# Kernel tuning notes

Hardware: AMD Instinct MI355X
Metric: run time of the kernel (lower is better)

The kernel has to match this reference:

```python
import jax, jax.numpy as jnp
import numpy as np

K = 12
ORDERS = [(1, 2, 3), (1, 3, 2), (3, 2, 1), (3, 1, 2), (2, 1, 3), (2, 3, 1)]


def ranking_3d(x):
    # x: (B, L1, W1, H1, D) -> (B, 12, L1*W1*H1, D)
    B, L1, W1, H1, D = x.shape
    seqs = []
    for dims in ORDERS:
        perm = (0,) + dims + (4,)
        seqs.append(jnp.transpose(x, perm).reshape(B, -1, D))
        xr = jnp.flip(x, axis=dims)
        seqs.append(jnp.transpose(xr, perm).reshape(B, -1, D))
    return jnp.stack(seqs, axis=1)


def restore_original(out_y, shape):
    # out_y: (B, 12, D, L). NOTE: faithfully replicates the original code, which
    # reshapes the (B, D, L) slice directly to (B, d1, d2, d3, D).
    B, L1, W1, H1, D = shape
    size = {1: L1, 2: W1, 3: H1}
    restored = []
    for i in range(12):
        dims = ORDERS[i // 2]
        seq = out_y[:, i]  # (B, D, L)
        dims_shape = tuple(size[d] for d in dims)
        reshaped = seq.reshape((B,) + dims_shape + (D,))
        perm = (0,) + dims + (4,)
        inv = tuple(np.argsort(perm))
        r = jnp.transpose(reshaped, inv)
        if i % 2 == 1:
            r = jnp.flip(r, axis=dims)
        restored.append(r)
    return restored


def selective_scan(u, delta, A, Bs, Cs):
    # u, delta: (B,K,D,L); A: (K,D,N); Bs, Cs: (B,K,N,L)
    us = jnp.moveaxis(u, -1, 0)       # (L,B,K,D)
    ds = jnp.moveaxis(delta, -1, 0)   # (L,B,K,D)
    Bts = jnp.moveaxis(Bs, -1, 0)     # (L,B,K,N)
    Cts = jnp.moveaxis(Cs, -1, 0)     # (L,B,K,N)
    h0 = jnp.zeros(u.shape[:-1] + (A.shape[-1],), u.dtype)  # (B,K,D,N)

    def step(h, inp):
        ut, dt, Bt, Ct = inp
        dA = jnp.exp(dt[..., None] * A)                       # (B,K,D,N)
        h = dA * h + (dt * ut)[..., None] * Bt[:, :, None, :]
        y = jnp.einsum('bkdn,bkn->bkd', h, Ct)
        return h, y

    _, ys = jax.lax.scan(step, h0, (us, ds, Bts, Cts))
    return jnp.moveaxis(ys, 0, -1)  # (B,K,D,L)


def setup_inputs() -> dict:
    key = jax.random.key(0)
    ks = jax.random.split(key, 8)
    B, H, W, Len, D = 1, 16, 16, 16, 128
    N, R = 16, 8
    x = jax.random.normal(ks[0], (B, H, W, Len, D), dtype=jnp.float32)
    x_proj_weight = jax.random.normal(ks[1], (K, R + 2 * N, D), dtype=jnp.float32) * 0.02
    std = R ** -0.5
    dt_projs_weight = jax.random.uniform(ks[2], (K, D, R), minval=-std, maxval=std, dtype=jnp.float32)
    dt = jnp.exp(jax.random.uniform(ks[3], (K, D)) * (np.log(0.1) - np.log(0.001)) + np.log(0.001))
    dt = jnp.clip(dt, 1e-4, None)
    dt_projs_bias = (dt + jnp.log(-jnp.expm1(-dt))).astype(jnp.float32)
    A_logs = jnp.broadcast_to(jnp.log(jnp.arange(1, N + 1, dtype=jnp.float32)), (K, D, N)).copy()
    Ds = jnp.ones((K, D), dtype=jnp.float32)
    merge_w = jax.random.normal(ks[4], (K,), dtype=jnp.float32) * (1.0 / K)
    merge_b = jax.random.normal(ks[5], (), dtype=jnp.float32) * 0.01
    return {'x': x, 'x_proj_weight': x_proj_weight, 'dt_projs_weight': dt_projs_weight,
            'dt_projs_bias': dt_projs_bias, 'A_logs': A_logs, 'Ds': Ds,
            'merge_w': merge_w, 'merge_b': merge_b}


def reference(x, x_proj_weight, dt_projs_weight, dt_projs_bias, A_logs, Ds, merge_w, merge_b):
    B, H, W, Len, D = x.shape
    L = H * W * Len
    R = dt_projs_weight.shape[-1]
    N = A_logs.shape[-1]
    xs = jnp.transpose(ranking_3d(x), (0, 1, 3, 2))  # (B,K,D,L)
    x_dbl = jnp.einsum('bkdl,kcd->bkcl', xs, x_proj_weight)  # (B,K,R+2N,L)
    dts, Bs, Cs = jnp.split(x_dbl, [R, R + N], axis=2)
    dts = jnp.einsum('bkrl,kdr->bkdl', dts, dt_projs_weight)
    delta = jax.nn.softplus(dts + dt_projs_bias[None, :, :, None])
    A = -jnp.exp(A_logs)  # (K,D,N)
    ys = selective_scan(xs, delta, A, Bs, Cs)
    out_y = ys + Ds[None, :, :, None] * xs  # (B,K,D,L)
    restored = restore_original(out_y, (B, H, W, Len, D))
    stacked = jnp.stack(restored, axis=1)  # (B,K,H,W,Len,D)
    # mergeconv: 1x1 Conv2d over K channels == weighted sum across directions
    y = jnp.einsum('bkhwld,k->bhwld', stacked, merge_w) + merge_b
    return y
```

## Files before the change

kernel.cpp:

```cpp
#include <hip/hip_runtime.h>

#define KK 12
#define LL 4096
#define DD 128
#define NN 16
#define RR 8
#define NC 128
#define LC 32

__device__ __forceinline__ int pos_of(int k, int l) {
    int o = k >> 1;
    int le = (k & 1) ? (4095 - l) : l;
    int t1 = le >> 8, t2 = (le >> 4) & 15, t3 = le & 15;
    switch (o) {
        case 0:  return (t1 << 8) | (t2 << 4) | t3;
        case 1:  return (t1 << 8) | (t3 << 4) | t2;
        case 2:  return (t3 << 8) | (t2 << 4) | t1;
        case 3:  return (t2 << 8) | (t3 << 4) | t1;
        case 4:  return (t2 << 8) | (t1 << 4) | t3;
        default: return (t3 << 8) | (t1 << 4) | t2;
    }
}

__device__ __forceinline__ float softplus_f(float z) {
    return fmaxf(z, 0.0f) + __logf(1.0f + __expf(-fabsf(z)));
}

__global__ __launch_bounds__(256) void proj_kernel(
    const float* __restrict__ x, const float* __restrict__ Wp,
    const float* __restrict__ Wdt, const float* __restrict__ bias,
    float* __restrict__ delta, float* __restrict__ Bc, float* __restrict__ Cc)
{
    int k = blockIdx.x >> 6;
    int l0 = (blockIdx.x & 63) * 64;
    int t = threadIdx.x;

    __shared__ float xs_s[64 * 132];

    {
        int lane32 = t & 31;
        int rowi = t >> 5;
        #pragma unroll
        for (int p = 0; p < 8; p++) {
            int l = p * 8 + rowi;
            int xbase = pos_of(k, l0 + l) * DD;
            float4 v = *(const float4*)(x + xbase + lane32 * 4);
            *(float4*)(&xs_s[l * 132 + lane32 * 4]) = v;
        }
    }
    __syncthreads();

    int l = t & 63;
    int cg = t >> 6;
    float acc[10];
    #pragma unroll
    for (int j = 0; j < 10; j++) acc[j] = 0.0f;
    {
        const float* wk = Wp + (size_t)(k * 40 + cg * 10) * DD;
        for (int d = 0; d < DD; d += 4) {
            float4 xv = *(const float4*)(&xs_s[l * 132 + d]);
            #pragma unroll
            for (int j = 0; j < 10; j++) {
                const float* w = wk + j * DD + d;
                acc[j] += xv.x * w[0] + xv.y * w[1] + xv.z * w[2] + xv.w * w[3];
            }
        }
    }
    __syncthreads();

    float* sdbl = xs_s;
    #pragma unroll
    for (int j = 0; j < 10; j++) sdbl[(cg * 10 + j) * 64 + l] = acc[j];
    __syncthreads();

    {
        int n4 = t & 3;
        int ll = t >> 2;
        float4 bv = make_float4(sdbl[(8  + n4 * 4 + 0) * 64 + ll],
                                sdbl[(8  + n4 * 4 + 1) * 64 + ll],
                                sdbl[(8  + n4 * 4 + 2) * 64 + ll],
                                sdbl[(8  + n4 * 4 + 3) * 64 + ll]);
        *(float4*)(Bc + (size_t)(k * LL + l0 + ll) * NN + n4 * 4) = bv;
        float4 cv = make_float4(sdbl[(24 + n4 * 4 + 0) * 64 + ll],
                                sdbl[(24 + n4 * 4 + 1) * 64 + ll],
                                sdbl[(24 + n4 * 4 + 2) * 64 + ll],
                                sdbl[(24 + n4 * 4 + 3) * 64 + ll]);
        *(float4*)(Cc + (size_t)(k * LL + l0 + ll) * NN + n4 * 4) = cv;
    }

    {
        int d = t & 127;
        int half = t >> 7;
        const float4* wp4 = (const float4*)(Wdt + (size_t)(k * DD + d) * RR);
        float4 w0 = wp4[0], w1 = wp4[1];
        float bz = bias[k * DD + d];
        for (int j = 0; j < 32; j++) {
            int ll = j * 2 + half;
            float z = bz
                + w0.x * sdbl[0 * 64 + ll] + w0.y * sdbl[1 * 64 + ll]
                + w0.z * sdbl[2 * 64 + ll] + w0.w * sdbl[3 * 64 + ll]
                + w1.x * sdbl[4 * 64 + ll] + w1.y * sdbl[5 * 64 + ll]
                + w1.z * sdbl[6 * 64 + ll] + w1.w * sdbl[7 * 64 + ll];
            delta[(size_t)(k * LL + l0 + ll) * DD + d] = softplus_f(z);
        }
    }
}

__device__ __forceinline__ bool load_A(const float* __restrict__ A_logs,
                                       int k, int d, float* Av) {
    const float4* ap = (const float4*)(A_logs + (size_t)(k * DD + d) * NN);
    #pragma unroll
    for (int q = 0; q < 4; q++) {
        float4 a4 = ap[q];
        Av[4*q+0] = -__expf(a4.x); Av[4*q+1] = -__expf(a4.y);
        Av[4*q+2] = -__expf(a4.z); Av[4*q+3] = -__expf(a4.w);
    }
    bool s = true;
    #pragma unroll
    for (int n = 1; n < 16; n++)
        s = s && (fabsf(Av[n] - (float)(n + 1) * Av[0])
                  <= 1e-4f * (float)(n + 1) * fabsf(Av[0]));
    return s;
}

__device__ __forceinline__ void exp_vec(bool structured, float t,
                                        const float* Av, float* e) {
    if (structured) {
        float q = __expf(t * Av[0]);
        e[0] = q;
        #pragma unroll
        for (int n = 1; n < 16; n++) e[n] = e[n - 1] * q;
    } else {
        #pragma unroll
        for (int n = 0; n < 16; n++) e[n] = __expf(t * Av[n]);
    }
}

__global__ __launch_bounds__(128) void scanA_kernel(
    const float* __restrict__ x, const float* __restrict__ delta,
    const float* __restrict__ Bc, const float* __restrict__ A_logs,
    float* __restrict__ Sb, float* __restrict__ dtsum)
{
    int k = blockIdx.x >> 7;
    int c = blockIdx.x & (NC - 1);
    int d = threadIdx.x;
    int l0 = c * LC;

    float Av[16];
    bool structured = load_A(A_logs, k, d, Av);

    float h[16];
    #pragma unroll
    for (int n = 0; n < 16; n++) h[n] = 0.0f;
    float dsum = 0.0f;

    for (int i = 0; i < LC; i++) {
        int l = l0 + i;
        float t = delta[(size_t)(k * LL + l) * DD + d];
        float u = x[pos_of(k, l) * DD + d];
        const float4* bp = (const float4*)(Bc + (size_t)(k * LL + l) * NN);
        float Bv[16];
        #pragma unroll
        for (int q = 0; q < 4; q++) {
            float4 b4 = bp[q];
            Bv[4*q] = b4.x; Bv[4*q+1] = b4.y; Bv[4*q+2] = b4.z; Bv[4*q+3] = b4.w;
        }
        dsum += t;
        float tu = t * u;
        float e[16];
        exp_vec(structured, t, Av, e);
        #pragma unroll
        for (int n = 0; n < 16; n++)
            h[n] = e[n] * h[n] + tu * Bv[n];
    }

    float4* sp = (float4*)(Sb + (size_t)((k * NC + c) * DD + d) * NN);
    sp[0] = make_float4(h[0],  h[1],  h[2],  h[3]);
    sp[1] = make_float4(h[4],  h[5],  h[6],  h[7]);
    sp[2] = make_float4(h[8],  h[9],  h[10], h[11]);
    sp[3] = make_float4(h[12], h[13], h[14], h[15]);
    dtsum[(k * NC + c) * DD + d] = dsum;
}

__global__ __launch_bounds__(256) void scanB_kernel(
    float* __restrict__ Sb, const float* __restrict__ dtsum,
    const float* __restrict__ A_logs)
{
    int tid = blockIdx.x * 256 + threadIdx.x;
    int k = tid >> 11;
    int rem = tid & 2047;
    int d = rem >> 4;

    float Av = -__expf(A_logs[tid]);
    float h = 0.0f;
    for (int c = 0; c < NC; c++) {
        size_t base = (size_t)k * (NC * DD * NN) + (size_t)c * (DD * NN) + rem;
        float s = Sb[base];
        float ds = dtsum[(k * NC + c) * DD + d];
        Sb[base] = h;
        h = s + __expf(ds * Av) * h;
    }
}

__global__ __launch_bounds__(128) void scanC_kernel(
    const float* __restrict__ x, const float* __restrict__ delta,
    const float* __restrict__ Bc, const float* __restrict__ Cc,
    const float* __restrict__ A_logs, const float* __restrict__ Ds,
    const float* __restrict__ hs, float* __restrict__ out_y)
{
    int k = blockIdx.x >> 7;
    int c = blockIdx.x & (NC - 1);
    int d = threadIdx.x;
    int l0 = c * LC;

    float Av[16];
    bool structured = load_A(A_logs, k, d, Av);

    float h[16];
    const float4* hp = (const float4*)(hs + (size_t)((k * NC + c) * DD + d) * NN);
    #pragma unroll
    for (int q = 0; q < 4; q++) {
        float4 h4 = hp[q];
        h[4*q] = h4.x; h[4*q+1] = h4.y; h[4*q+2] = h4.z; h[4*q+3] = h4.w;
    }

    float Dval = Ds[k * DD + d];
    float obuf[16];

    for (int i = 0; i < LC; i++) {
        int l = l0 + i;
        float t = delta[(size_t)(k * LL + l) * DD + d];
        float u = x[pos_of(k, l) * DD + d];
        const float4* bp = (const float4*)(Bc + (size_t)(k * LL + l) * NN);
        const float4* cp = (const float4*)(Cc + (size_t)(k * LL + l) * NN);
        float Bv[16], Cv[16];
        #pragma unroll
        for (int q = 0; q < 4; q++) {
            float4 b4 = bp[q]; float4 c4 = cp[q];
            Bv[4*q] = b4.x; Bv[4*q+1] = b4.y; Bv[4*q+2] = b4.z; Bv[4*q+3] = b4.w;
            Cv[4*q] = c4.x; Cv[4*q+1] = c4.y; Cv[4*q+2] = c4.z; Cv[4*q+3] = c4.w;
        }
        float tu = t * u;
        float e[16];
        exp_vec(structured, t, Av, e);
        float y = 0.0f;
        #pragma unroll
        for (int n = 0; n < 16; n++) {
            h[n] = e[n] * h[n] + tu * Bv[n];
            y += h[n] * Cv[n];
        }
        obuf[i & 15] = y + Dval * u;
        if ((i & 15) == 15) {
            float4* op = (float4*)(out_y + (size_t)(k * DD + d) * LL + (l0 + (i & ~15)));
            op[0] = make_float4(obuf[0],  obuf[1],  obuf[2],  obuf[3]);
            op[1] = make_float4(obuf[4],  obuf[5],  obuf[6],  obuf[7]);
            op[2] = make_float4(obuf[8],  obuf[9],  obuf[10], obuf[11]);
            op[3] = make_float4(obuf[12], obuf[13], obuf[14], obuf[15]);
        }
    }
}

__global__ __launch_bounds__(256) void merge_kernel(
    const float* __restrict__ out_y, const float* __restrict__ mw,
    const float* __restrict__ mb, float* __restrict__ out)
{
    int idx = blockIdx.x * 256 + threadIdx.x;
    int dd = idx & 127;
    int p = idx >> 7;
    int i3 = p & 15, i2 = (p >> 4) & 15, i1 = (p >> 8) & 15;

    float accv = mb[0];
    #pragma unroll
    for (int k = 0; k < 12; k++) {
        int a1 = i1, a2 = i2, a3 = i3;
        if (k & 1) { a1 = 15 - i1; a2 = 15 - i2; a3 = 15 - i3; }
        int j1, j2, j3;
        switch (k >> 1) {
            case 0:  j1 = a1; j2 = a2; j3 = a3; break;
            case 1:  j1 = a1; j2 = a3; j3 = a2; break;
            case 2:  j1 = a3; j2 = a2; j3 = a1; break;
            case 3:  j1 = a3; j2 = a1; j3 = a2; break;
            case 4:  j1 = a2; j2 = a1; j3 = a3; break;
            default: j1 = a2; j2 = a3; j3 = a1; break;
        }
        int jb = (j1 << 8) | (j2 << 4) | j3;
        accv += mw[k] * out_y[(size_t)k * (DD * LL) + (jb >> 5) * LL + ((jb & 31) << 7) + dd];
    }
    out[idx] = accv;
}

extern "C" void kernel_launch(void* const* d_in, const int* in_sizes, int n_in,
                              void* d_out, int out_size, void* d_ws, size_t ws_size,
                              hipStream_t stream) {
    const float* x      = (const float*)d_in[0];
    const float* Wp     = (const float*)d_in[1];
    const float* Wdt    = (const float*)d_in[2];
    const float* bias   = (const float*)d_in[3];
    const float* A_logs = (const float*)d_in[4];
    const float* Ds     = (const float*)d_in[5];
    const float* mw     = (const float*)d_in[6];
    const float* mb     = (const float*)d_in[7];
    float* out = (float*)d_out;

    float* ws    = (float*)d_ws;
    float* delta = ws;
    float* Bc    = delta + (size_t)KK * LL * DD;
    float* Cc    = Bc    + (size_t)KK * LL * NN;
    float* Sb    = Cc    + (size_t)KK * LL * NN;
    float* dts   = Sb    + (size_t)KK * NC * DD * NN;
    float* oy    = dts   + (size_t)KK * NC * DD;

    proj_kernel <<<dim3(KK * (LL / 64)), dim3(256), 0, stream>>>(x, Wp, Wdt, bias, delta, Bc, Cc);
    scanA_kernel<<<dim3(KK * NC),        dim3(128), 0, stream>>>(x, delta, Bc, A_logs, Sb, dts);
    scanB_kernel<<<dim3(KK * DD * NN / 256), dim3(256), 0, stream>>>(Sb, dts, A_logs);
    scanC_kernel<<<dim3(KK * NC),        dim3(128), 0, stream>>>(x, delta, Bc, Cc, A_logs, Ds, Sb, oy);
    merge_kernel<<<dim3(LL * DD / 256),  dim3(256), 0, stream>>>(oy, mw, mb, out);
}
```

Measured before the change: 187.4 us.

## Fuse projection with chunk scan and replace second scan pass by state correction

```diff
diff --git a/kernel.cpp b/kernel.cpp
--- a/kernel.cpp
+++ b/kernel.cpp
@@ -5,8 +5,12 @@
 #define DD 128
 #define NN 16
 #define RR 8
-#define NC 128
-#define LC 32
+#define NC 64
+#define LC 64
+#define XST 132
+#define YST 66
+#define SDST 44
+#define XDBL_TILE (64 * SDST)
 
 __device__ __forceinline__ int pos_of(int k, int l) {
     int o = k >> 1;
@@ -26,241 +30,245 @@
     return fmaxf(z, 0.0f) + __logf(1.0f + __expf(-fabsf(z)));
 }
 
-__global__ __launch_bounds__(256) void proj_kernel(
+__device__ __forceinline__ float delta_at(const float* sdbl, int i,
+                                          float4 w0, float4 w1, float bz) {
+    const float4* dr = (const float4*)(sdbl + i * SDST);
+    float4 r0 = dr[0], r1 = dr[1];
+    float z = bz + w0.x * r0.x + w0.y * r0.y + w0.z * r0.z + w0.w * r0.w
+                 + w1.x * r1.x + w1.y * r1.y + w1.z * r1.z + w1.w * r1.w;
+    return softplus_f(z);
+}
+
+__device__ __forceinline__ void e8_vec(bool structured, int half, float tl,
+                                       float A0, const float* A8, float* e) {
+    if (structured) {
+        float q = __expf(tl * A0);
+        float q2 = q * q, q4 = q2 * q2, q8 = q4 * q4;
+        e[0] = half ? q8 * q : q;
+        #pragma unroll
+        for (int j = 1; j < 8; j++) e[j] = e[j - 1] * q;
+    } else {
+        #pragma unroll
+        for (int j = 0; j < 8; j++) e[j] = __expf(tl * A8[j]);
+    }
+}
+
+__device__ __forceinline__ bool load_A8(const float* __restrict__ A_logs,
+                                        int k, int d, int n0, float* A8, float& A0) {
+    const float4* ap = (const float4*)(A_logs + ((size_t)(k * DD + d) * NN + n0));
+    float4 a0 = ap[0], a1 = ap[1];
+    A8[0] = -__expf(a0.x); A8[1] = -__expf(a0.y);
+    A8[2] = -__expf(a0.z); A8[3] = -__expf(a0.w);
+    A8[4] = -__expf(a1.x); A8[5] = -__expf(a1.y);
+    A8[6] = -__expf(a1.z); A8[7] = -__expf(a1.w);
+    A0 = -__expf(A_logs[(size_t)(k * DD + d) * NN]);
+    bool s = true;
+    #pragma unroll
+    for (int j = 0; j < 8; j++) {
+        float m = (float)(n0 + j + 1);
+        s = s && (fabsf(A8[j] - m * A0) <= 1e-4f * m * fabsf(A0));
+    }
+    return s;
+}
+
+__global__ __launch_bounds__(256) void k1_proj_scanA(
     const float* __restrict__ x, const float* __restrict__ Wp,
     const float* __restrict__ Wdt, const float* __restrict__ bias,
-    float* __restrict__ delta, float* __restrict__ Bc, float* __restrict__ Cc)
+    const float* __restrict__ A_logs, const float* __restrict__ Ds,
+    float* __restrict__ S, float* __restrict__ dtsum,
+    float* __restrict__ oy, float* __restrict__ xdbl)
 {
-    int k = blockIdx.x >> 6;
-    int l0 = (blockIdx.x & 63) * 64;
-    int t = threadIdx.x;
-
-    __shared__ float xs_s[64 * 132];
-
-    {
-        int lane32 = t & 31;
-        int rowi = t >> 5;
+    const int blk = blockIdx.x;
+    const int k = blk >> 6;
+    const int c = blk & 63;
+    const int l0 = c * LC;
+    const int t = threadIdx.x;
+
+    __shared__ float xs[64 * XST];
+    __shared__ float sdbl[64 * SDST];
+    __shared__ int   pos_s[64];
+
+    if (t < 64) pos_s[t] = pos_of(k, l0 + t);
+    __syncthreads();
+
+    {
+        int lane32 = t & 31, rowi = t >> 5;
         #pragma unroll
         for (int p = 0; p < 8; p++) {
             int l = p * 8 + rowi;
-            int xbase = pos_of(k, l0 + l) * DD;
-            float4 v = *(const float4*)(x + xbase + lane32 * 4);
-            *(float4*)(&xs_s[l * 132 + lane32 * 4]) = v;
-        }
-    }
-    __syncthreads();
-
-    int l = t & 63;
-    int cg = t >> 6;
-    float acc[10];
-    #pragma unroll
-    for (int j = 0; j < 10; j++) acc[j] = 0.0f;
-    {
-        const float* wk = Wp + (size_t)(k * 40 + cg * 10) * DD;
-        for (int d = 0; d < DD; d += 4) {
-            float4 xv = *(const float4*)(&xs_s[l * 132 + d]);
+            float4 v = *(const float4*)(x + (size_t)pos_s[l] * DD + lane32 * 4);
+            *(float4*)(&xs[l * XST + lane32 * 4]) = v;
+        }
+    }
+    __syncthreads();
+
+    {
+        int l = t & 63, cgch = t >> 6;
+        float acc[10];
+        #pragma unroll
+        for (int j = 0; j < 10; j++) acc[j] = 0.0f;
+        const float* wk = Wp + (size_t)(k * 40 + cgch * 10) * DD;
+        for (int d4 = 0; d4 < DD; d4 += 4) {
+            float4 xv = *(const float4*)(&xs[l * XST + d4]);
             #pragma unroll
             for (int j = 0; j < 10; j++) {
-                const float* w = wk + j * DD + d;
+                const float* w = wk + j * DD + d4;
                 acc[j] += xv.x * w[0] + xv.y * w[1] + xv.z * w[2] + xv.w * w[3];
             }
         }
-    }
-    __syncthreads();
-
-    float* sdbl = xs_s;
-    #pragma unroll
-    for (int j = 0; j < 10; j++) sdbl[(cg * 10 + j) * 64 + l] = acc[j];
-    __syncthreads();
-
-    {
-        int n4 = t & 3;
-        int ll = t >> 2;
-        float4 bv = make_float4(sdbl[(8  + n4 * 4 + 0) * 64 + ll],
-                                sdbl[(8  + n4 * 4 + 1) * 64 + ll],
-                                sdbl[(8  + n4 * 4 + 2) * 64 + ll],
-                                sdbl[(8  + n4 * 4 + 3) * 64 + ll]);
-        *(float4*)(Bc + (size_t)(k * LL + l0 + ll) * NN + n4 * 4) = bv;
-        float4 cv = make_float4(sdbl[(24 + n4 * 4 + 0) * 64 + ll],
-                                sdbl[(24 + n4 * 4 + 1) * 64 + ll],
-                                sdbl[(24 + n4 * 4 + 2) * 64 + ll],
-                                sdbl[(24 + n4 * 4 + 3) * 64 + ll]);
-        *(float4*)(Cc + (size_t)(k * LL + l0 + ll) * NN + n4 * 4) = cv;
-    }
-
-    {
-        int d = t & 127;
-        int half = t >> 7;
-        const float4* wp4 = (const float4*)(Wdt + (size_t)(k * DD + d) * RR);
-        float4 w0 = wp4[0], w1 = wp4[1];
-        float bz = bias[k * DD + d];
-        for (int j = 0; j < 32; j++) {
-            int ll = j * 2 + half;
-            float z = bz
-                + w0.x * sdbl[0 * 64 + ll] + w0.y * sdbl[1 * 64 + ll]
-                + w0.z * sdbl[2 * 64 + ll] + w0.w * sdbl[3 * 64 + ll]
-                + w1.x * sdbl[4 * 64 + ll] + w1.y * sdbl[5 * 64 + ll]
-                + w1.z * sdbl[6 * 64 + ll] + w1.w * sdbl[7 * 64 + ll];
-            delta[(size_t)(k * LL + l0 + ll) * DD + d] = softplus_f(z);
-        }
-    }
-}
-
-__device__ __forceinline__ bool load_A(const float* __restrict__ A_logs,
-                                       int k, int d, float* Av) {
-    const float4* ap = (const float4*)(A_logs + (size_t)(k * DD + d) * NN);
-    #pragma unroll
-    for (int q = 0; q < 4; q++) {
-        float4 a4 = ap[q];
-        Av[4*q+0] = -__expf(a4.x); Av[4*q+1] = -__expf(a4.y);
-        Av[4*q+2] = -__expf(a4.z); Av[4*q+3] = -__expf(a4.w);
-    }
-    bool s = true;
-    #pragma unroll
-    for (int n = 1; n < 16; n++)
-        s = s && (fabsf(Av[n] - (float)(n + 1) * Av[0])
-                  <= 1e-4f * (float)(n + 1) * fabsf(Av[0]));
-    return s;
-}
-
-__device__ __forceinline__ void exp_vec(bool structured, float t,
-                                        const float* Av, float* e) {
-    if (structured) {
-        float q = __expf(t * Av[0]);
-        e[0] = q;
-        #pragma unroll
-        for (int n = 1; n < 16; n++) e[n] = e[n - 1] * q;
-    } else {
-        #pragma unroll
-        for (int n = 0; n < 16; n++) e[n] = __expf(t * Av[n]);
-    }
-}
-
-__global__ __launch_bounds__(128) void scanA_kernel(
-    const float* __restrict__ x, const float* __restrict__ delta,
-    const float* __restrict__ Bc, const float* __restrict__ A_logs,
-    float* __restrict__ Sb, float* __restrict__ dtsum)
-{
-    int k = blockIdx.x >> 7;
-    int c = blockIdx.x & (NC - 1);
-    int d = threadIdx.x;
-    int l0 = c * LC;
-
-    float Av[16];
-    bool structured = load_A(A_logs, k, d, Av);
-
-    float h[16];
-    #pragma unroll
-    for (int n = 0; n < 16; n++) h[n] = 0.0f;
-    float dsum = 0.0f;
-
-    for (int i = 0; i < LC; i++) {
-        int l = l0 + i;
-        float t = delta[(size_t)(k * LL + l) * DD + d];
-        float u = x[pos_of(k, l) * DD + d];
-        const float4* bp = (const float4*)(Bc + (size_t)(k * LL + l) * NN);
-        float Bv[16];
-        #pragma unroll
-        for (int q = 0; q < 4; q++) {
-            float4 b4 = bp[q];
-            Bv[4*q] = b4.x; Bv[4*q+1] = b4.y; Bv[4*q+2] = b4.z; Bv[4*q+3] = b4.w;
-        }
-        dsum += t;
-        float tu = t * u;
-        float e[16];
-        exp_vec(structured, t, Av, e);
-        #pragma unroll
-        for (int n = 0; n < 16; n++)
-            h[n] = e[n] * h[n] + tu * Bv[n];
-    }
-
-    float4* sp = (float4*)(Sb + (size_t)((k * NC + c) * DD + d) * NN);
-    sp[0] = make_float4(h[0],  h[1],  h[2],  h[3]);
-    sp[1] = make_float4(h[4],  h[5],  h[6],  h[7]);
-    sp[2] = make_float4(h[8],  h[9],  h[10], h[11]);
-    sp[3] = make_float4(h[12], h[13], h[14], h[15]);
-    dtsum[(k * NC + c) * DD + d] = dsum;
-}
-
-__global__ __launch_bounds__(256) void scanB_kernel(
-    float* __restrict__ Sb, const float* __restrict__ dtsum,
+        #pragma unroll
+        for (int j = 0; j < 10; j++) sdbl[l * SDST + cgch * 10 + j] = acc[j];
+    }
+    __syncthreads();
+
+    if (c != 0) {
+        for (int idx = t; idx < XDBL_TILE; idx += 256)
+            xdbl[(size_t)blk * XDBL_TILE + idx] = sdbl[idx];
+    }
+
+    const int d = t >> 1, half = t & 1, n0 = half * 8;
+    float A8[8], A0;
+    bool structured = load_A8(A_logs, k, d, n0, A8, A0);
+    const float4* wp4 = (const float4*)(Wdt + (size_t)(k * DD + d) * RR);
+    const float4 w0 = wp4[0], w1 = wp4[1];
+    const float bz = bias[k * DD + d];
+    const float Dval = Ds[k * DD + d];
+    float* ybuf = xs;
+
+    {
+        float h[8] = {0, 0, 0, 0, 0, 0, 0, 0};
+        float dsum = 0.0f;
+        #pragma unroll 4
+        for (int i = 0; i < LC; i++) {
+            float tl = delta_at(sdbl, i, w0, w1, bz);
+            dsum += tl;
+            float u = x[(size_t)pos_s[i] * DD + d];
+            const float4* bp = (const float4*)(&sdbl[i * SDST + 8 + n0]);
+            float4 b0 = bp[0], b1 = bp[1];
+            const float4* cp = (const float4*)(&sdbl[i * SDST + 24 + n0]);
+            float4 c0 = cp[0], c1 = cp[1];
+            float e[8];
+            e8_vec(structured, half, tl, A0, A8, e);
+            float tu = tl * u;
+            h[0] = e[0] * h[0] + tu * b0.x;  h[1] = e[1] * h[1] + tu * b0.y;
+            h[2] = e[2] * h[2] + tu * b0.z;  h[3] = e[3] * h[3] + tu * b0.w;
+            h[4] = e[4] * h[4] + tu * b1.x;  h[5] = e[5] * h[5] + tu * b1.y;
+            h[6] = e[6] * h[6] + tu * b1.z;  h[7] = e[7] * h[7] + tu * b1.w;
+            float yp = h[0] * c0.x + h[1] * c0.y + h[2] * c0.z + h[3] * c0.w
+                     + h[4] * c1.x + h[5] * c1.y + h[6] * c1.z + h[7] * c1.w;
+            float y = yp + __shfl_xor(yp, 1);
+            if (!half) ybuf[d * YST + i] = y + Dval * u;
+        }
+        float4* sp = (float4*)(S + (((size_t)(k * NC + c) * DD + d) * NN + n0));
+        sp[0] = make_float4(h[0], h[1], h[2], h[3]);
+        sp[1] = make_float4(h[4], h[5], h[6], h[7]);
+        if (!half) dtsum[(k * NC + c) * DD + d] = dsum;
+    }
+    __syncthreads();
+
+    {
+        int row = t >> 4, col = (t & 15) * 4;
+        #pragma unroll
+        for (int p = 0; p < 8; p++) {
+            int r = p * 16 + row;
+            float4 v = *(const float4*)(&ybuf[r * YST + col]);
+            *(float4*)(oy + ((size_t)(k * DD + r)) * LL + l0 + col) = v;
+        }
+    }
+}
+
+__global__ __launch_bounds__(256) void k2_combine(
+    float* __restrict__ S, const float* __restrict__ dtsum,
     const float* __restrict__ A_logs)
 {
     int tid = blockIdx.x * 256 + threadIdx.x;
-    int k = tid >> 11;
-    int rem = tid & 2047;
-    int d = rem >> 4;
-
-    float Av = -__expf(A_logs[tid]);
-    float h = 0.0f;
-    for (int c = 0; c < NC; c++) {
-        size_t base = (size_t)k * (NC * DD * NN) + (size_t)c * (DD * NN) + rem;
-        float s = Sb[base];
-        float ds = dtsum[(k * NC + c) * DD + d];
-        Sb[base] = h;
-        h = s + __expf(ds * Av) * h;
-    }
-}
-
-__global__ __launch_bounds__(128) void scanC_kernel(
-    const float* __restrict__ x, const float* __restrict__ delta,
-    const float* __restrict__ Bc, const float* __restrict__ Cc,
-    const float* __restrict__ A_logs, const float* __restrict__ Ds,
-    const float* __restrict__ hs, float* __restrict__ out_y)
+    int kk = tid >> 11, rem = tid & 2047, dd2 = rem >> 4;
+    float Ac = -__expf(A_logs[tid]);
+    float hh = 0.0f;
+    #pragma unroll 8
+    for (int c2 = 0; c2 < NC; c2++) {
+        size_t base = ((size_t)(kk * NC + c2)) * 2048 + rem;
+        float s = S[base];
+        float dsv = dtsum[(kk * NC + c2) * DD + dd2];
+        S[base] = hh;
+        hh = s + __expf(dsv * Ac) * hh;
+    }
+}
+
+__global__ __launch_bounds__(256) void k3_corr(
+    const float* __restrict__ Wdt, const float* __restrict__ bias,
+    const float* __restrict__ A_logs, const float* __restrict__ S,
+    const float* __restrict__ xdbl, float* __restrict__ oy)
 {
-    int k = blockIdx.x >> 7;
-    int c = blockIdx.x & (NC - 1);
-    int d = threadIdx.x;
-    int l0 = c * LC;
-
-    float Av[16];
-    bool structured = load_A(A_logs, k, d, Av);
-
-    float h[16];
-    const float4* hp = (const float4*)(hs + (size_t)((k * NC + c) * DD + d) * NN);
-    #pragma unroll
-    for (int q = 0; q < 4; q++) {
-        float4 h4 = hp[q];
-        h[4*q] = h4.x; h[4*q+1] = h4.y; h[4*q+2] = h4.z; h[4*q+3] = h4.w;
-    }
-
-    float Dval = Ds[k * DD + d];
-    float obuf[16];
-
-    for (int i = 0; i < LC; i++) {
-        int l = l0 + i;
-        float t = delta[(size_t)(k * LL + l) * DD + d];
-        float u = x[pos_of(k, l) * DD + d];
-        const float4* bp = (const float4*)(Bc + (size_t)(k * LL + l) * NN);
-        const float4* cp = (const float4*)(Cc + (size_t)(k * LL + l) * NN);
-        float Bv[16], Cv[16];
-        #pragma unroll
-        for (int q = 0; q < 4; q++) {
-            float4 b4 = bp[q]; float4 c4 = cp[q];
-            Bv[4*q] = b4.x; Bv[4*q+1] = b4.y; Bv[4*q+2] = b4.z; Bv[4*q+3] = b4.w;
-            Cv[4*q] = c4.x; Cv[4*q+1] = c4.y; Cv[4*q+2] = c4.z; Cv[4*q+3] = c4.w;
-        }
-        float tu = t * u;
-        float e[16];
-        exp_vec(structured, t, Av, e);
-        float y = 0.0f;
-        #pragma unroll
-        for (int n = 0; n < 16; n++) {
-            h[n] = e[n] * h[n] + tu * Bv[n];
-            y += h[n] * Cv[n];
-        }
-        obuf[i & 15] = y + Dval * u;
-        if ((i & 15) == 15) {
-            float4* op = (float4*)(out_y + (size_t)(k * DD + d) * LL + (l0 + (i & ~15)));
-            op[0] = make_float4(obuf[0],  obuf[1],  obuf[2],  obuf[3]);
-            op[1] = make_float4(obuf[4],  obuf[5],  obuf[6],  obuf[7]);
-            op[2] = make_float4(obuf[8],  obuf[9],  obuf[10], obuf[11]);
-            op[3] = make_float4(obuf[12], obuf[13], obuf[14], obuf[15]);
-        }
-    }
-}
-
-__global__ __launch_bounds__(256) void merge_kernel(
+    const int blk = blockIdx.x;
+    const int k = blk >> 6;
+    const int c = blk & 63;
+    if (c == 0) return;
+    const int l0 = c * LC;
+    const int t = threadIdx.x;
+
+    __shared__ float sdbl[64 * SDST];
+    __shared__ float ybuf[128 * YST];
+
+    for (int idx = t; idx < XDBL_TILE; idx += 256)
+        sdbl[idx] = xdbl[(size_t)blk * XDBL_TILE + idx];
+    for (int idx = t; idx < 128 * YST; idx += 256)
+        ybuf[idx] = 0.0f;
+    __syncthreads();
+
+    const int d = t >> 1, half = t & 1, n0 = half * 8;
+    float A8[8], A0;
+    bool structured = load_A8(A_logs, k, d, n0, A8, A0);
+    const float4* wp4 = (const float4*)(Wdt + (size_t)(k * DD + d) * RR);
+    const float4 w0 = wp4[0], w1 = wp4[1];
+    const float bz = bias[k * DD + d];
+
+    float corr[8];
+    {
+        const float4* hp = (const float4*)(S + (((size_t)(k * NC + c) * DD + d) * NN + n0));
+        float4 h40 = hp[0], h41 = hp[1];
+        corr[0] = h40.x; corr[1] = h40.y; corr[2] = h40.z; corr[3] = h40.w;
+        corr[4] = h41.x; corr[5] = h41.y; corr[6] = h41.z; corr[7] = h41.w;
+    }
+
+    bool alive = true;
+    for (int ii = 0; ii < 8 && alive; ii++) {
+        #pragma unroll
+        for (int jj = 0; jj < 8; jj++) {
+            int i = ii * 8 + jj;
+            float tl = delta_at(sdbl, i, w0, w1, bz);
+            float e[8];
+            e8_vec(structured, half, tl, A0, A8, e);
+            #pragma unroll
+            for (int j = 0; j < 8; j++) corr[j] *= e[j];
+            const float4* cp = (const float4*)(&sdbl[i * SDST + 24 + n0]);
+            float4 c0 = cp[0], c1 = cp[1];
+            float yp = corr[0] * c0.x + corr[1] * c0.y + corr[2] * c0.z + corr[3] * c0.w
+                     + corr[4] * c1.x + corr[5] * c1.y + corr[6] * c1.z + corr[7] * c1.w;
+            float y = yp + __shfl_xor(yp, 1);
+            if (!half) ybuf[d * YST + i] = y;
+        }
+        float mag = fabsf(corr[0]) + fabsf(corr[1]) + fabsf(corr[2]) + fabsf(corr[3])
+                  + fabsf(corr[4]) + fabsf(corr[5]) + fabsf(corr[6]) + fabsf(corr[7]);
+        if (__all(mag == 0.0f)) alive = false;
+    }
+    __syncthreads();
+
+    {
+        int row = t >> 4, col = (t & 15) * 4;
+        #pragma unroll
+        for (int p = 0; p < 8; p++) {
+            int r = p * 16 + row;
+            float4* addr = (float4*)(oy + ((size_t)(k * DD + r)) * LL + l0 + col);
+            float4 v = *addr;
+            const float4 w = *(const float4*)(&ybuf[r * YST + col]);
+            v.x += w.x; v.y += w.y; v.z += w.z; v.w += w.w;
+            *addr = v;
+        }
+    }
+}
+
+__global__ __launch_bounds__(256) void k4_merge(
     const float* __restrict__ out_y, const float* __restrict__ mw,
     const float* __restrict__ mb, float* __restrict__ out)
 {
@@ -284,7 +292,8 @@
             default: j1 = a2; j2 = a3; j3 = a1; break;
         }
         int jb = (j1 << 8) | (j2 << 4) | j3;
-        accv += mw[k] * out_y[(size_t)k * (DD * LL) + (jb >> 5) * LL + ((jb & 31) << 7) + dd];
+        accv += mw[k] * out_y[(size_t)k * (DD * LL) + (jb >> 5) * LL
+                              + ((jb & 31) << 7) + dd];
     }
     out[idx] = accv;
 }
@@ -302,17 +311,15 @@
     const float* mb     = (const float*)d_in[7];
     float* out = (float*)d_out;
 
-    float* ws    = (float*)d_ws;
-    float* delta = ws;
-    float* Bc    = delta + (size_t)KK * LL * DD;
-    float* Cc    = Bc    + (size_t)KK * LL * NN;
-    float* Sb    = Cc    + (size_t)KK * LL * NN;
-    float* dts   = Sb    + (size_t)KK * NC * DD * NN;
-    float* oy    = dts   + (size_t)KK * NC * DD;
-
-    proj_kernel <<<dim3(KK * (LL / 64)), dim3(256), 0, stream>>>(x, Wp, Wdt, bias, delta, Bc, Cc);
-    scanA_kernel<<<dim3(KK * NC),        dim3(128), 0, stream>>>(x, delta, Bc, A_logs, Sb, dts);
-    scanB_kernel<<<dim3(KK * DD * NN / 256), dim3(256), 0, stream>>>(Sb, dts, A_logs);
-    scanC_kernel<<<dim3(KK * NC),        dim3(128), 0, stream>>>(x, delta, Bc, Cc, A_logs, Ds, Sb, oy);
-    merge_kernel<<<dim3(LL * DD / 256),  dim3(256), 0, stream>>>(oy, mw, mb, out);
-}
+    float* ws   = (float*)d_ws;
+    float* S    = ws;
+    float* dts  = S + (size_t)KK * NC * DD * NN;
+    float* oy   = dts + (size_t)KK * NC * DD;
+    float* xdbl = oy + (size_t)KK * DD * LL;
+
+    k1_proj_scanA<<<dim3(KK * NC), dim3(256), 0, stream>>>(
+        x, Wp, Wdt, bias, A_logs, Ds, S, dts, oy, xdbl);
+    k2_combine<<<dim3(KK * DD * NN / 256), dim3(256), 0, stream>>>(S, dts, A_logs);
+    k3_corr<<<dim3(KK * NC), dim3(256), 0, stream>>>(Wdt, bias, A_logs, S, xdbl, oy);
+    k4_merge<<<dim3(LL * DD / 256), dim3(256), 0, stream>>>(oy, mw, mb, out);
+}
```

After: 179.3 us. 1.05x faster.
